# Performance work log

Hardware: AMD Instinct MI355X
Metric: run time of the kernel (lower is better)

The kernel has to match this reference:

```python
import jax, jax.numpy as jnp
import numpy as np

HEADS, DIM_HEAD = 8, 64
SCALE = DIM_HEAD ** -0.5
LAMDA1, LAMDA2 = 5.0, 5.0


def setup_inputs() -> dict:
    B, N, M = 32, 1536, 80  # N = 32*48 spatial tokens, M = max_boxes
    QD, KD, VD = 320, 768, 768
    inner = HEADS * DIM_HEAD
    ks = jax.random.split(jax.random.key(0), 11)
    return {
        "x": jax.random.normal(ks[0], (B, N, QD), jnp.float32),
        "key": jax.random.normal(ks[1], (B, M, KD), jnp.float32),
        "value": jax.random.normal(ks[2], (B, M, VD), jnp.float32),
        "mask": jax.random.randint(ks[3], (B, M), 0, 2).astype(bool),
        "perl_box_masking_map": jax.random.normal(ks[4], (B, N, M), jnp.float32),
        "perl_road_masking_map": jax.random.normal(ks[5], (B, 1, N), jnp.float32),
        "Wq": jax.random.normal(ks[6], (inner, QD), jnp.float32) * 0.02,
        "Wk": jax.random.normal(ks[7], (inner, KD), jnp.float32) * 0.02,
        "Wv": jax.random.normal(ks[8], (inner, VD), jnp.float32) * 0.02,
        "Wo": jax.random.normal(ks[9], (QD, inner), jnp.float32) * 0.02,
        "bo": jnp.zeros((QD,), jnp.float32),
    }


def reference(x, key, value, mask, perl_box_masking_map, perl_road_masking_map, Wq, Wk, Wv, Wo, bo):
    B, N, _ = x.shape
    M = key.shape[1]
    H, C = HEADS, DIM_HEAD
    # QKV projections (torch Linear: y = x @ W.T)
    q = (x @ Wq.T).reshape(B, N, H, C)
    k = (key @ Wk.T).reshape(B, M, H, C)
    v = (value @ Wv.T).reshape(B, M, H, C)
    # attention scores with scale, key mask, and two additive bias maps
    sim = jnp.einsum('bnhc,bmhc->bhnm', q, k) * SCALE  # (B, H, N, M)
    neg = -jnp.finfo(sim.dtype).max
    sim = jnp.where(mask[:, None, None, :], sim, neg)  # mask fill BEFORE bias adds, as in torch
    sim = sim + LAMDA1 * perl_box_masking_map[:, None, :, :]
    road = jnp.swapaxes(perl_road_masking_map, 1, 2)  # (B, N, 1) -> broadcast over key axis
    sim = sim + LAMDA2 * road[:, None, :, :]
    attn = jax.nn.softmax(sim, axis=-1)
    out = jnp.einsum('bhnm,bmhc->bnhc', attn, v).reshape(B, N, H * C)
    return out @ Wo.T + bo  # dropout is identity in eval
```

## Files before the change

### kernel.cpp

```cpp
#include <hip/hip_runtime.h>
#include <hip/hip_bf16.h>

typedef __attribute__((ext_vector_type(8))) short short8;
typedef __attribute__((ext_vector_type(4))) short short4v;
typedef __attribute__((ext_vector_type(4))) float floatx4;
typedef __attribute__((ext_vector_type(2))) unsigned uint2v;
typedef unsigned short u16;

#define NB 32
#define NN 1536
#define NM 80
#define NH 8
#define NC 64
#define NINNER 512
#define NQD 320
#define NKD 768

__device__ __forceinline__ float bf2f(u16 u) {
    union { unsigned i; float f; } x; x.i = ((unsigned)u) << 16; return x.f;
}
__device__ __forceinline__ u16 f2bf(float f) {
    unsigned u = __float_as_uint(f);
    unsigned r = (u + 0x7FFFu + ((u >> 16) & 1u)) >> 16;
    return (u16)r;
}
__device__ __forceinline__ unsigned cvt_pk_bf16(float lo, float hi) {
    unsigned r;
    asm("v_cvt_pk_bf16_f32 %0, %1, %2" : "=v"(r) : "v"(lo), "v"(hi));
    return r;
}
__device__ __forceinline__ short8 cvt8(const float* __restrict__ p) {
    float4 a = ((const float4*)p)[0];
    float4 b = ((const float4*)p)[1];
    short8 r;
    r[0] = (short)f2bf(a.x); r[1] = (short)f2bf(a.y);
    r[2] = (short)f2bf(a.z); r[3] = (short)f2bf(a.w);
    r[4] = (short)f2bf(b.x); r[5] = (short)f2bf(b.y);
    r[6] = (short)f2bf(b.z); r[7] = (short)f2bf(b.w);
    return r;
}
__device__ __forceinline__ void gload16(const u16* g, u16* l) {
    __builtin_amdgcn_global_load_lds(
        (const __attribute__((address_space(1))) unsigned int*)g,
        (__attribute__((address_space(3))) unsigned int*)l, 16, 0, 0);
}

__global__ __launch_bounds__(256) void prep(const u16* __restrict__ x,
                                            const unsigned char* __restrict__ raw,
                                            int* __restrict__ flag,
                                            float* __restrict__ maskbias) {
    if (blockIdx.x == 0) {
        __shared__ int cnt;
        if (threadIdx.x == 0) cnt = 0;
        __syncthreads();
        int c = 0;
        for (int i = threadIdx.x; i < 8192; i += 256) {
            unsigned e = (x[i] >> 7) & 0xFF;
            if (e >= 0xA0) c++;
        }
        atomicAdd(&cnt, c);
        __syncthreads();
        if (threadIdx.x == 0) *flag = (cnt > 64) ? 1 : 0;
    } else {
        __shared__ int c_bf, c_f32, c_u8;
        if (threadIdx.x == 0) { c_bf = 0; c_f32 = 0; c_u8 = 0; }
        __syncthreads();
        for (int i = threadIdx.x; i < NB * NM; i += 256) {
            unsigned char v = raw[i];
            if (v == 0x3F && (i & 3) == 1) atomicAdd(&c_bf, 1);
            if (v == 0x3F && (i & 3) == 3) atomicAdd(&c_f32, 1);
            if (v != 0 && (i & 3) != 0) atomicAdd(&c_u8, 1);
        }
        __syncthreads();
        int md;
        if (c_bf > 0) md = 2;
        else if (c_f32 > 0) md = 3;
        else if (c_u8 > 0) md = 1;
        else md = 0;
        for (int i = threadIdx.x; i < NB * NM; i += 256) {
            bool on;
            if (md == 2) on = ((const u16*)raw)[i] != 0;
            else if (md == 3) on = ((const float*)raw)[i] != 0.0f;
            else if (md == 1) on = raw[i] != 0;
            else on = ((const int*)raw)[i] != 0;
            maskbias[i] = on ? 0.0f : -3.4028234663852886e38f;
        }
    }
}

struct ConvSeg { const void* src; u16* dst; long nreal; long nblk; };
struct ConvArgs { ConvSeg s[7]; };

__global__ __launch_bounds__(256) void conv_batch(ConvArgs a, const int* __restrict__ flag) {
    const int f = *flag;
    long b = blockIdx.x; int seg = 0;
    while (seg < 7 && b >= a.s[seg].nblk) { b -= a.s[seg].nblk; seg++; }
    if (seg >= 7) return;
    const long idx = b * 2048 + threadIdx.x * 8;
    u16* dst = a.s[seg].dst;
    if (idx >= a.s[seg].nreal) { *(short8*)(dst + idx) = (short8)0; return; }
    if (f) *(short8*)(dst + idx) = cvt8((const float*)a.s[seg].src + idx);
    else   *(short8*)(dst + idx) = *(const short8*)((const u16*)a.s[seg].src + idx);
}

template <bool OUT_DYN, bool BIAS>
__device__ __forceinline__ void gemm_body(const u16* __restrict__ A,
                                          const u16* __restrict__ B,
                                          const void* __restrict__ bias,
                                          void* __restrict__ C,
                                          int bx, int by, int Nreal, int K, int f,
                                          u16* As, u16* Bs) {
    const int tid = threadIdx.x;
    const int wave = tid >> 6, lane = tid & 63;
    const int l16 = lane & 15, quad = lane >> 4;
    const int wr = wave >> 1, wc = wave & 1;
    const int bm0 = bx * 128, bn0 = by * 128;

    const int r0 = tid >> 2, c0 = tid & 3;
    const int sc = c0 ^ ((r0 >> 1) & 3);
    const u16* Ag = A + (size_t)(bm0 + r0) * K + sc * 8;
    const u16* Bg = B + (size_t)(bn0 + r0) * K + sc * 8;

    const int swz = (l16 >> 1) & 3;
    floatx4 acc[4][4];
#pragma unroll
    for (int i = 0; i < 4; ++i)
#pragma unroll
        for (int n = 0; n < 4; ++n) acc[i][n] = (floatx4)0.0f;

    {
        u16* AsW = As + wave * 512;
        u16* BsW = Bs + wave * 512;
        gload16(Ag, AsW);                  gload16(Ag + (size_t)64 * K, AsW + 2048);
        gload16(Bg, BsW);                  gload16(Bg + (size_t)64 * K, BsW + 2048);
    }
    __syncthreads();

    int cur = 0;
    for (int kk = 0; kk < K; kk += 32) {
        if (kk + 32 < K) {
            u16* AsW = As + (cur ^ 1) * 4096 + wave * 512;
            u16* BsW = Bs + (cur ^ 1) * 4096 + wave * 512;
            gload16(Ag + kk + 32, AsW);
            gload16(Ag + (size_t)64 * K + kk + 32, AsW + 2048);
            gload16(Bg + kk + 32, BsW);
            gload16(Bg + (size_t)64 * K + kk + 32, BsW + 2048);
        }
        const u16* Asr = As + cur * 4096;
        const u16* Bsr = Bs + cur * 4096;
        short8 af[4], bf[4];
#pragma unroll
        for (int i = 0; i < 4; ++i)
            af[i] = *(const short8*)&Asr[(wr * 64 + i * 16 + l16) * 32 + ((quad ^ swz) * 8)];
#pragma unroll
        for (int n = 0; n < 4; ++n)
            bf[n] = *(const short8*)&Bsr[(wc * 64 + n * 16 + l16) * 32 + ((quad ^ swz) * 8)];
#pragma unroll
        for (int i = 0; i < 4; ++i)
#pragma unroll
            for (int n = 0; n < 4; ++n)
                acc[i][n] = __builtin_amdgcn_mfma_f32_16x16x32_bf16(af[i], bf[n], acc[i][n], 0, 0, 0);
        __syncthreads();
        cur ^= 1;
    }

#pragma unroll
    for (int n = 0; n < 4; ++n) {
        const int col = bn0 + wc * 64 + n * 16 + l16;
        if (col < Nreal) {
            float badd = 0.0f;
            if (BIAS) badd = f ? ((const float*)bias)[col] : bf2f(((const u16*)bias)[col]);
#pragma unroll
            for (int i = 0; i < 4; ++i)
#pragma unroll
                for (int r = 0; r < 4; ++r) {
                    const int row = bm0 + wr * 64 + i * 16 + quad * 4 + r;
                    const float val = acc[i][n][r] + badd;
                    if (OUT_DYN && f) ((float*)C)[(size_t)row * Nreal + col] = val;
                    else              ((u16*)C)[(size_t)row * Nreal + col] = f2bf(val);
                }
        }
    }
}

struct GemmRoles {
    const u16* A[3]; const u16* B[3]; u16* C[3];
    int mblk[3]; int kdim[3]; int start[3];
};

__global__ __launch_bounds__(256) void gemm_qkv(GemmRoles g) {
    __shared__ __align__(16) u16 As[2 * 128 * 32];
    __shared__ __align__(16) u16 Bs[2 * 128 * 32];
    const int id = blockIdx.x;
    const int role = (id >= g.start[1]) + (id >= g.start[2]);
    const int rid = id - g.start[role];
    const int mb = g.mblk[role];
    const int bx = rid % mb, by = rid / mb;
    gemm_body<false, false>(g.A[role], g.B[role], nullptr, g.C[role],
                            bx, by, NINNER, g.kdim[role], 0, As, Bs);
}

__global__ __launch_bounds__(256) void gemm_out(const u16* __restrict__ A,
                                                const u16* __restrict__ B,
                                                const void* __restrict__ bias,
                                                void* __restrict__ C,
                                                const int* __restrict__ flag) {
    __shared__ __align__(16) u16 As[2 * 128 * 32];
    __shared__ __align__(16) u16 Bs[2 * 128 * 32];
    const int f = *flag;
    gemm_body<true, true>(A, B, bias, C, blockIdx.x, blockIdx.y, NQD, NINNER, f, As, Bs);
}

__global__ __launch_bounds__(256) void transpose_v(const u16* __restrict__ v,
                                                   u16* __restrict__ vT) {
    int b = blockIdx.x >> 3, h = blockIdx.x & 7;
    const u16* src = v + (size_t)b * NM * NINNER + h * NC;
    u16* o = vT + (size_t)(b * NH + h) * NC * 128;
    for (int idx = threadIdx.x; idx < NC * 128; idx += 256) {
        int c = idx >> 7, m = idx & 127;
        u16 val = (m < NM) ? src[(size_t)m * NINNER + c] : (u16)0;
        o[c * 128 + ((((m >> 3) ^ (c & 7))) << 3) + (m & 7)] = val;
    }
}

__global__ __launch_bounds__(256) void attn_kernel(const u16* __restrict__ q,
                                                   const u16* __restrict__ k,
                                                   const u16* __restrict__ vT,
                                                   const float* __restrict__ maskbias,
                                                   const void* __restrict__ box,
                                                   const void* __restrict__ road,
                                                   u16* __restrict__ attno,
                                                   const int* __restrict__ flag) {
    const int f = *flag;
    const int n0 = blockIdx.x * 64;
    const int h = blockIdx.y;
    const int b = blockIdx.z;
    const int tid = threadIdx.x;
    const int wave = tid >> 6, lane = tid & 63;
    const int l16 = lane & 15, quad = lane >> 4;

    __shared__ __align__(16) u16 K_lds[80 * 64];
    __shared__ __align__(16) u16 V_lds[64 * 128];
    __shared__ __align__(16) u16 p_lds[64][104];

    {
        const int row0 = tid >> 3;
        const int cswz = (tid & 7) ^ (row0 & 7);
        const u16* kg = k + ((size_t)b * NM + row0) * NINNER + h * NC + cswz * 8;
        u16* kw = K_lds + wave * 512;
        gload16(kg, kw);
        gload16(kg + (size_t)32 * NINNER, kw + 2048);
        if (wave < 2)
            gload16(kg + (size_t)64 * NINNER, kw + 4096);
    }
    {
        const u16* vg = vT + (size_t)(b * NH + h) * NC * 128 + tid * 8;
        u16* vw = V_lds + wave * 512;
#pragma unroll
        for (int i = 0; i < 4; ++i)
            gload16(vg + i * 2048, vw + i * 2048);
    }

    const int n = n0 + 16 * wave + l16;
    const size_t qrow = (size_t)(b * NN + n) * NINNER + h * NC;
    short8 qa[2];
    qa[0] = *(const short8*)(q + qrow + 0 + quad * 8);
    qa[1] = *(const short8*)(q + qrow + 32 + quad * 8);
    const size_t boxbase = ((size_t)b * NN + n) * NM;
    floatx4 bx4[5]; short4v bxh[5]; floatx4 mb4[5];
    float roadf = 0.0f; u16 roadh = 0;
    if (f) {
#pragma unroll
        for (int mt = 0; mt < 5; ++mt)
            bx4[mt] = *(const floatx4*)((const float*)box + boxbase + 16 * mt + 4 * quad);
        roadf = ((const float*)road)[(size_t)b * NN + n];
    } else {
#pragma unroll
        for (int mt = 0; mt < 5; ++mt)
            bxh[mt] = *(const short4v*)((const u16*)box + boxbase + 16 * mt + 4 * quad);
        roadh = ((const u16*)road)[(size_t)b * NN + n];
    }
#pragma unroll
    for (int mt = 0; mt < 5; ++mt)
        mb4[mt] = *(const floatx4*)(maskbias + b * NM + 16 * mt + 4 * quad);

    const float roadv = 5.0f * (f ? roadf : bf2f(roadh));
    floatx4 cb[5];
#pragma unroll
    for (int mt = 0; mt < 5; ++mt)
#pragma unroll
        for (int r = 0; r < 4; ++r) {
            const float boxv = f ? bx4[mt][r] : bf2f((u16)bxh[mt][r]);
            cb[mt][r] = mb4[mt][r] + 5.0f * boxv + roadv;
        }

    __syncthreads();

    const int rsw = l16 & 7;
    floatx4 s[5];
#pragma unroll
    for (int i = 0; i < 5; ++i) s[i] = (floatx4)0.0f;
#pragma unroll
    for (int kk2 = 0; kk2 < 2; ++kk2)
#pragma unroll
        for (int mt = 0; mt < 5; ++mt) {
            short8 kfr = *(const short8*)&K_lds[(mt * 16 + l16) * 64 + (((kk2 * 4 + quad) ^ rsw) * 8)];
            s[mt] = __builtin_amdgcn_mfma_f32_16x16x32_bf16(kfr, qa[kk2], s[mt], 0, 0, 0);
        }

#pragma unroll
    for (int mt = 0; mt < 5; ++mt)
#pragma unroll
        for (int r = 0; r < 4; ++r)
            s[mt][r] = s[mt][r] * 0.125f + cb[mt][r];

    float mx;
    {
        float t0 = fmaxf(fmaxf(s[0][0], s[0][1]), fmaxf(s[0][2], s[0][3]));
        float t1 = fmaxf(fmaxf(s[1][0], s[1][1]), fmaxf(s[1][2], s[1][3]));
        float t2 = fmaxf(fmaxf(s[2][0], s[2][1]), fmaxf(s[2][2], s[2][3]));
        float t3 = fmaxf(fmaxf(s[3][0], s[3][1]), fmaxf(s[3][2], s[3][3]));
        float t4 = fmaxf(fmaxf(s[4][0], s[4][1]), fmaxf(s[4][2], s[4][3]));
        mx = fmaxf(fmaxf(fmaxf(t0, t1), fmaxf(t2, t3)), t4);
    }
    mx = fmaxf(mx, __shfl_xor(mx, 16));
    mx = fmaxf(mx, __shfl_xor(mx, 32));
    float sum = 0.0f;
#pragma unroll
    for (int mt = 0; mt < 5; ++mt)
#pragma unroll
        for (int r = 0; r < 4; ++r) {
            const float p = __expf(s[mt][r] - mx);
            s[mt][r] = p;
            sum += p;
        }
    sum += __shfl_xor(sum, 16);
    sum += __shfl_xor(sum, 32);
    const float inv = 1.0f / sum;

#pragma unroll
    for (int mt = 0; mt < 5; ++mt) {
        uint2v pk;
        pk[0] = cvt_pk_bf16(s[mt][0] * inv, s[mt][1] * inv);
        pk[1] = cvt_pk_bf16(s[mt][2] * inv, s[mt][3] * inv);
        *(uint2v*)&p_lds[16 * wave + l16][16 * mt + 4 * quad] = pk;
    }
    if (quad < 2) *(short8*)&p_lds[16 * wave + l16][80 + 8 * quad] = (short8)0;
    asm volatile("s_waitcnt lgkmcnt(0)" ::: "memory");
    __builtin_amdgcn_sched_barrier(0);

    floatx4 o[4];
#pragma unroll
    for (int i = 0; i < 4; ++i) o[i] = (floatx4)0.0f;
#pragma unroll
    for (int kt = 0; kt < 3; ++kt) {
        short8 pb = *(const short8*)&p_lds[16 * wave + l16][kt * 32 + quad * 8];
#pragma unroll
        for (int nt = 0; nt < 4; ++nt) {
            short8 vfr = *(const short8*)&V_lds[(nt * 16 + l16) * 128 + (((kt * 4 + quad) ^ rsw) * 8)];
            o[nt] = __builtin_amdgcn_mfma_f32_16x16x32_bf16(pb, vfr, o[nt], 0, 0, 0);
        }
    }

#pragma unroll
    for (int nt = 0; nt < 4; ++nt) {
#pragma unroll
        for (int r = 0; r < 4; ++r) {
            int nr = n0 + 16 * wave + quad * 4 + r;
            attno[((size_t)b * NN + nr) * NINNER + h * NC + nt * 16 + l16] = f2bf(o[nt][r]);
        }
    }
}

extern "C" void kernel_launch(void* const* d_in, const int* in_sizes, int n_in,
                              void* d_out, int out_size, void* d_ws, size_t ws_size,
                              hipStream_t stream) {
    (void)in_sizes; (void)n_in; (void)out_size; (void)ws_size;
    const void* x    = d_in[0];
    const void* key  = d_in[1];
    const void* val  = d_in[2];
    const unsigned char* mask = (const unsigned char*)d_in[3];
    const void* box  = d_in[4];
    const void* road = d_in[5];
    const void* Wq   = d_in[6];
    const void* Wk   = d_in[7];
    const void* Wv   = d_in[8];
    const void* Wo   = d_in[9];
    const void* bo   = d_in[10];

    char* ws = (char*)d_ws;
    size_t off = 0;
    auto carve = [&](size_t bytes) {
        char* p = ws + off;
        off += (bytes + 255) & ~(size_t)255;
        return p;
    };
    int* flag   = (int*)carve(256);
    u16* q_ws   = (u16*)carve((size_t)NB * NN * NINNER * 2);
    u16* k_ws   = (u16*)carve((size_t)NB * NM * NINNER * 2);
    u16* v_ws   = (u16*)carve((size_t)NB * NM * NINNER * 2);
    u16* vT_ws  = (u16*)carve((size_t)NB * NH * NC * 128 * 2);
    u16* ao_ws  = (u16*)carve((size_t)NB * NN * NINNER * 2);
    u16* x_bf   = ao_ws;
    u16* key_bf = (u16*)carve((size_t)NB * NM * NKD * 2);
    u16* val_bf = (u16*)carve((size_t)NB * NM * NKD * 2);
    u16* Wq_bf  = (u16*)carve((size_t)NINNER * NQD * 2);
    u16* Wk_bf  = (u16*)carve((size_t)NINNER * NKD * 2);
    u16* Wv_bf  = (u16*)carve((size_t)NINNER * NKD * 2);
    u16* WoP_bf = (u16*)carve((size_t)384 * NINNER * 2);
    float* mb   = (float*)carve((size_t)NB * NM * 4);

    prep<<<2, 256, 0, stream>>>((const u16*)x, mask, flag, mb);

    ConvArgs ca;
    ca.s[0] = { x,     x_bf,   (long)NB * NN * NQD, (long)NB * NN * NQD / 2048 };
    ca.s[1] = { key,   key_bf, (long)NB * NM * NKD, (long)NB * NM * NKD / 2048 };
    ca.s[2] = { val,   val_bf, (long)NB * NM * NKD, (long)NB * NM * NKD / 2048 };
    ca.s[3] = { Wq,    Wq_bf,  (long)NINNER * NQD,  (long)NINNER * NQD / 2048 };
    ca.s[4] = { Wk,    Wk_bf,  (long)NINNER * NKD,  (long)NINNER * NKD / 2048 };
    ca.s[5] = { Wv,    Wv_bf,  (long)NINNER * NKD,  (long)NINNER * NKD / 2048 };
    ca.s[6] = { Wo,    WoP_bf, (long)NQD * NINNER,  (long)384 * NINNER / 2048 };
    long totblk = 0;
    for (int i = 0; i < 7; ++i) totblk += ca.s[i].nblk;
    conv_batch<<<(int)totblk, 256, 0, stream>>>(ca, flag);

    GemmRoles g;
    g.A[0] = key_bf; g.B[0] = Wk_bf; g.C[0] = k_ws; g.mblk[0] = NB * NM / 128; g.kdim[0] = NKD;
    g.A[1] = val_bf; g.B[1] = Wv_bf; g.C[1] = v_ws; g.mblk[1] = NB * NM / 128; g.kdim[1] = NKD;
    g.A[2] = x_bf;   g.B[2] = Wq_bf; g.C[2] = q_ws; g.mblk[2] = NB * NN / 128; g.kdim[2] = NQD;
    g.start[0] = 0;
    g.start[1] = g.mblk[0] * 4;
    g.start[2] = g.start[1] + g.mblk[1] * 4;
    int gtot = g.start[2] + g.mblk[2] * 4;
    gemm_qkv<<<gtot, 256, 0, stream>>>(g);

    transpose_v<<<NB * NH, 256, 0, stream>>>(v_ws, vT_ws);
    attn_kernel<<<dim3(NN / 64, NH, NB), 256, 0, stream>>>(
        q_ws, k_ws, vT_ws, mb, box, road, ao_ws, flag);
    gemm_out<<<dim3(NB * NN / 128, 384 / 128), 256, 0, stream>>>(
        ao_ws, WoP_bf, bo, d_out, flag);
}
```

Measured before the change: 298.1 us.

## Triple-buffer GEMM shared-memory tiles with vmcnt-based waits and single barrier

Changes the GEMM main loop from double buffering with two syncthreads per step to a three-stage ring buffer. Prefetch runs two steps ahead, completion is tracked with explicit s_waitcnt vmcnt, and there is one s_barrier per step, issued after the LDS reads. The goal is to hide global-to-LDS load latency and cut barrier stalls. It raises LDS use per block from 32KB to 48KB, which may lower occupancy, and it relies on the exact count of outstanding loads per stage being correct.

```diff
diff --git a/kernel.cpp b/kernel.cpp
--- a/kernel.cpp
+++ b/kernel.cpp
@@ -128,26 +128,27 @@
 #pragma unroll
         for (int n = 0; n < 4; ++n) acc[i][n] = (floatx4)0.0f;
 
-    {
-        u16* AsW = As + wave * 512;
-        u16* BsW = Bs + wave * 512;
-        gload16(Ag, AsW);                  gload16(Ag + (size_t)64 * K, AsW + 2048);
-        gload16(Bg, BsW);                  gload16(Bg + (size_t)64 * K, BsW + 2048);
-    }
-    __syncthreads();
-
-    int cur = 0;
-    for (int kk = 0; kk < K; kk += 32) {
-        if (kk + 32 < K) {
-            u16* AsW = As + (cur ^ 1) * 4096 + wave * 512;
-            u16* BsW = Bs + (cur ^ 1) * 4096 + wave * 512;
-            gload16(Ag + kk + 32, AsW);
-            gload16(Ag + (size_t)64 * K + kk + 32, AsW + 2048);
-            gload16(Bg + kk + 32, BsW);
-            gload16(Bg + (size_t)64 * K + kk + 32, BsW + 2048);
-        }
-        const u16* Asr = As + cur * 4096;
-        const u16* Bsr = Bs + cur * 4096;
+    const int nstep = K >> 5;
+    auto stage = [&](int t, int bi) {
+        u16* AsW = As + bi * 4096 + wave * 512;
+        u16* BsW = Bs + bi * 4096 + wave * 512;
+        gload16(Ag + t * 32, AsW);
+        gload16(Ag + (size_t)64 * K + t * 32, AsW + 2048);
+        gload16(Bg + t * 32, BsW);
+        gload16(Bg + (size_t)64 * K + t * 32, BsW + 2048);
+    };
+    stage(0, 0);
+    stage(1, 1);
+
+    int buf = 0;
+    for (int t = 0; t < nstep; ++t) {
+        if (t + 1 < nstep) asm volatile("s_waitcnt vmcnt(4)" ::: "memory");
+        else               asm volatile("s_waitcnt vmcnt(0)" ::: "memory");
+        __builtin_amdgcn_s_barrier();
+        __builtin_amdgcn_sched_barrier(0);
+
+        const u16* Asr = As + buf * 4096;
+        const u16* Bsr = Bs + buf * 4096;
         short8 af[4], bf[4];
 #pragma unroll
         for (int i = 0; i < 4; ++i)
@@ -155,13 +156,19 @@
 #pragma unroll
         for (int n = 0; n < 4; ++n)
             bf[n] = *(const short8*)&Bsr[(wc * 64 + n * 16 + l16) * 32 + ((quad ^ swz) * 8)];
+
+        if (t + 2 < nstep) {
+            const int bi = (buf == 0) ? 2 : buf - 1;
+            stage(t + 2, bi);
+        }
+
 #pragma unroll
         for (int i = 0; i < 4; ++i)
 #pragma unroll
             for (int n = 0; n < 4; ++n)
                 acc[i][n] = __builtin_amdgcn_mfma_f32_16x16x32_bf16(af[i], bf[n], acc[i][n], 0, 0, 0);
-        __syncthreads();
-        cur ^= 1;
+
+        buf = (buf == 2) ? 0 : buf + 1;
     }
 
 #pragma unroll
@@ -189,8 +196,8 @@
 };
 
 __global__ __launch_bounds__(256) void gemm_qkv(GemmRoles g) {
-    __shared__ __align__(16) u16 As[2 * 128 * 32];
-    __shared__ __align__(16) u16 Bs[2 * 128 * 32];
+    __shared__ __align__(16) u16 As[3 * 128 * 32];
+    __shared__ __align__(16) u16 Bs[3 * 128 * 32];
     const int id = blockIdx.x;
     const int role = (id >= g.start[1]) + (id >= g.start[2]);
     const int rid = id - g.start[role];
@@ -205,8 +212,8 @@
                                                 const void* __restrict__ bias,
                                                 void* __restrict__ C,
                                                 const int* __restrict__ flag) {
-    __shared__ __align__(16) u16 As[2 * 128 * 32];
-    __shared__ __align__(16) u16 Bs[2 * 128 * 32];
+    __shared__ __align__(16) u16 As[3 * 128 * 32];
+    __shared__ __align__(16) u16 Bs[3 * 128 * 32];
     const int f = *flag;
     gemm_body<true, true>(A, B, bias, C, blockIdx.x, blockIdx.y, NQD, NINNER, f, As, Bs);
 }
```

Measured after the change: 292.6 us. About the same (-1.9%).
